# Optimization experiments

Hardware: AMD Instinct MI355X
Metric: run time of the kernel (lower is better)

## Reference

```python
import jax, jax.numpy as jnp
import numpy as np

N = 50000       # nodes
E = 500000      # edges (before self loops)
IN = 256        # in_dim
HID = 128       # hidden
HEADS = 2       # GATv2 heads (concat=False -> head mean)
G = 64          # num graphs in batch
SLOPE = 0.2     # leaky_relu negative slope (PyG default)


def setup_inputs() -> dict:
    key = jax.random.key(0)
    ks = jax.random.split(key, 30)
    w = lambda k, shape: jax.random.normal(k, shape, jnp.float32) * 0.05
    inp = {
        "x": jax.random.normal(ks[0], (N, IN), jnp.float32),
        "edge_index": jax.random.randint(ks[1], (2, E), 0, N, dtype=jnp.int64),
        "batch": jnp.sort(jax.random.randint(ks[2], (N,), 0, G, dtype=jnp.int64)),
        # encoder MLP
        "enc_w1": w(ks[3], (HID, IN)),  "enc_b1": w(ks[4], (HID,)),
        "enc_w2": w(ks[5], (HID, HID)), "enc_b2": w(ks[6], (HID,)),
        # GATv2 conv1: lin_l, lin_r -> heads*out; att [H, C]; final bias [C]
        "c1_wl": w(ks[7], (HEADS * HID, HID)),  "c1_bl": w(ks[8], (HEADS * HID,)),
        "c1_wr": w(ks[9], (HEADS * HID, HID)),  "c1_br": w(ks[10], (HEADS * HID,)),
        "c1_att": w(ks[11], (HEADS, HID)),       "c1_bias": w(ks[12], (HID,)),
        # GATv2 conv2
        "c2_wl": w(ks[13], (HEADS * HID, HID)), "c2_bl": w(ks[14], (HEADS * HID,)),
        "c2_wr": w(ks[15], (HEADS * HID, HID)), "c2_br": w(ks[16], (HEADS * HID,)),
        "c2_att": w(ks[17], (HEADS, HID)),       "c2_bias": w(ks[18], (HID,)),
        # attentional pooling gate MLP
        "gate_w1": w(ks[19], (HID, HID)), "gate_b1": w(ks[20], (HID,)),
        "gate_w2": w(ks[21], (1, HID)),   "gate_b2": w(ks[22], (1,)),
        # head MLP
        "head_w1": w(ks[23], (HID, HID)), "head_b1": w(ks[24], (HID,)),
        "head_w2": w(ks[25], (2, HID)),   "head_b2": w(ks[26], (2,)),
    }
    return inp


def _gatv2(x, src, dst, wl, bl, wr, br, att, bias):
    """PyG GATv2Conv, heads=HEADS, concat=False (mean over heads)."""
    n = x.shape[0]
    xl = (x @ wl.T + bl).reshape(n, HEADS, HID)   # source transform
    xr = (x @ wr.T + br).reshape(n, HEADS, HID)   # target transform
    s = jax.nn.leaky_relu(xl[src] + xr[dst], SLOPE)          # [E,H,C]
    e = jnp.einsum('ehc,hc->eh', s, att)                      # [E,H]
    m = jax.ops.segment_max(e, dst, num_segments=n)
    a = jnp.exp(e - m[dst])
    a = a / (jax.ops.segment_sum(a, dst, num_segments=n)[dst] + 1e-16)
    out = jax.ops.segment_sum(a[:, :, None] * xl[src], dst, num_segments=n)
    return out.mean(axis=1) + bias                            # [N,C]


def _forward(x, edge_index, batch,
             enc_w1, enc_b1, enc_w2, enc_b2,
             c1_wl, c1_bl, c1_wr, c1_br, c1_att, c1_bias,
             c2_wl, c2_bl, c2_wr, c2_br, c2_att, c2_bias,
             gate_w1, gate_b1, gate_w2, gate_b2,
             head_w1, head_b1, head_w2, head_b2):
    n = x.shape[0]
    # add self loops (PyG GATv2Conv default add_self_loops=True)
    loop = jnp.arange(n, dtype=edge_index.dtype)
    src = jnp.concatenate([edge_index[0], loop])
    dst = jnp.concatenate([edge_index[1], loop])

    h = jax.nn.relu(x @ enc_w1.T + enc_b1)
    h = jax.nn.relu(h @ enc_w2.T + enc_b2)
    h = jax.nn.relu(_gatv2(h, src, dst, c1_wl, c1_bl, c1_wr, c1_br, c1_att, c1_bias))
    h = jax.nn.relu(_gatv2(h, src, dst, c2_wl, c2_bl, c2_wr, c2_br, c2_att, c2_bias))

    # attentional aggregation: segment-softmax gate over graphs
    gate = (jax.nn.relu(h @ gate_w1.T + gate_b1) @ gate_w2.T + gate_b2)[:, 0]  # [N]
    gm = jax.ops.segment_max(gate, batch, num_segments=G)
    ga = jnp.exp(gate - gm[batch])
    ga = ga / (jax.ops.segment_sum(ga, batch, num_segments=G)[batch] + 1e-16)
    g = jax.ops.segment_sum(ga[:, None] * h, batch, num_segments=G)  # [G,HID]

    out = jax.nn.relu(g @ head_w1.T + head_b1) @ head_w2.T + head_b2  # [G,2]
    # F.normalize(dim=1), eps=1e-12
    norm = jnp.linalg.norm(out, axis=1, keepdims=True)
    return out / jnp.maximum(norm, 1e-12)


def reference(x, edge_index, batch,
              enc_w1, enc_b1, enc_w2, enc_b2,
              c1_wl, c1_bl, c1_wr, c1_br, c1_att, c1_bias,
              c2_wl, c2_bl, c2_wr, c2_br, c2_att, c2_bias,
              gate_w1, gate_b1, gate_w2, gate_b2,
              head_w1, head_b1, head_w2, head_b2):
    return _forward(x, edge_index, batch,
                    enc_w1, enc_b1, enc_w2, enc_b2,
                    c1_wl, c1_bl, c1_wr, c1_br, c1_att, c1_bias,
                    c2_wl, c2_bl, c2_wr, c2_br, c2_att, c2_bias,
                    gate_w1, gate_b1, gate_w2, gate_b2,
                    head_w1, head_b1, head_w2, head_b2)
```

## Files before the change

### kernel.cpp

```cpp
#include <hip/hip_runtime.h>
#include <math.h>

#define CH 128
#define F2 256
#define NG 64
#define PS 16

typedef __attribute__((ext_vector_type(8))) short short8;
typedef __attribute__((ext_vector_type(4))) float f32x4;

__device__ inline ushort f2bf_t(float x) { return (ushort)(__float_as_uint(x) >> 16); }
__device__ inline ushort f2bf_r(float x) {
  uint u = __float_as_uint(x);
  return (ushort)((u + 0x7fffu + ((u >> 16) & 1u)) >> 16);
}
__device__ inline float bf2f(ushort h) { return __uint_as_float(((uint)h) << 16); }

struct WSpec { const float* src; ushort* hi; ushort* lo; int n; };
struct WPack { WSpec w[7]; };
__global__ __launch_bounds__(256) void split_weights(WPack p) {
  const WSpec s = p.w[blockIdx.y];
  for (int i = blockIdx.x * 256 + threadIdx.x; i < s.n; i += gridDim.x * 256) {
    const float v = s.src[i];
    if (s.lo) {
      const ushort h = f2bf_t(v);
      s.hi[i] = h;
      s.lo[i] = f2bf_t(v - bf2f(h));
    } else {
      s.hi[i] = f2bf_r(v);
    }
  }
}

template<int NT, int ACT, int AF32, int GATE, int SPLIT, int WSPLIT>
__global__ __launch_bounds__(NT * 128) void gemm_full(
    const void* __restrict__ Av, const ushort* __restrict__ Whi,
    const ushort* __restrict__ Wlo, const float* __restrict__ bias,
    const float* __restrict__ bias2, ushort* __restrict__ Cb0,
    ushort* __restrict__ Cb1, const float* __restrict__ w2,
    const float* __restrict__ b2, float* __restrict__ gate, int M, int K) {
  constexpr int Nn = NT * 64;
  constexpr int NTH = NT * 128;
  constexpr int ACF = AF32 ? (1024 / NTH) : 1;
  constexpr int ACB = AF32 ? 1 : ((512 + NTH - 1) / NTH);
  extern __shared__ ushort smem[];
  ushort* Ab = smem;
  ushort* Wh = smem + 128 * 40;
  ushort* Wl = WSPLIT ? (Wh + Nn * 40) : Wh;
  const int tid = threadIdx.x;
  const int lane = tid & 63, wid = tid >> 6;
  const int wm = wid / NT, wn = wid % NT;
  const int bm = blockIdx.x * 128;
  const int fr = lane & 15, fg = lane >> 4;

  f32x4 acc[4][4];
#pragma unroll
  for (int i = 0; i < 4; ++i)
#pragma unroll
    for (int j = 0; j < 4; ++j) acc[i][j] = (f32x4)0.f;

  float4 avf[ACF];
  short8 avb[ACB];
  short8 wvh[2], wvl[2];
  auto load_tiles = [&](int k0) {
    if constexpr (AF32) {
#pragma unroll
      for (int i2 = 0; i2 < ACF; ++i2) {
        const int c = tid + NTH * i2;
        const int row = c >> 3, kq = (c & 7) * 4;
        const int gr = bm + row;
        avf[i2] = (gr < M) ? *(const float4*)((const float*)Av + (size_t)gr * K + k0 + kq)
                           : make_float4(0.f, 0.f, 0.f, 0.f);
      }
    } else {
#pragma unroll
      for (int i2 = 0; i2 < ACB; ++i2) {
        const int c = tid + NTH * i2;
        if (c < 512) {
          const int row = c >> 2, kq = (c & 3) * 8;
          const int gr = bm + row;
          avb[i2] = (gr < M) ? *(const short8*)((const ushort*)Av + (size_t)gr * K + k0 + kq)
                             : (short8)0;
        }
      }
    }
#pragma unroll
    for (int i2 = 0; i2 < 2; ++i2) {
      const int c = tid + NTH * i2;
      const int row = c >> 2, kq = (c & 3) * 8;
      wvh[i2] = *(const short8*)(Whi + (size_t)row * K + k0 + kq);
      if constexpr (WSPLIT)
        wvl[i2] = *(const short8*)(Wlo + (size_t)row * K + k0 + kq);
    }
  };

  load_tiles(0);
  for (int k0 = 0; k0 < K; k0 += 32) {
    __syncthreads();
    if constexpr (AF32) {
#pragma unroll
      for (int i2 = 0; i2 < ACF; ++i2) {
        const int c = tid + NTH * i2;
        const int row = c >> 3, kq = (c & 7) * 4;
        const float4 v = avf[i2];
        ushort4 h;
        h.x = f2bf_r(v.x); h.y = f2bf_r(v.y); h.z = f2bf_r(v.z); h.w = f2bf_r(v.w);
        *(ushort4*)&Ab[row * 40 + kq] = h;
      }
    } else {
#pragma unroll
      for (int i2 = 0; i2 < ACB; ++i2) {
        const int c = tid + NTH * i2;
        if (c < 512) {
          const int row = c >> 2, kq = (c & 3) * 8;
          *(short8*)&Ab[row * 40 + kq] = avb[i2];
        }
      }
    }
#pragma unroll
    for (int i2 = 0; i2 < 2; ++i2) {
      const int c = tid + NTH * i2;
      const int row = c >> 2, kq = (c & 3) * 8;
      *(short8*)&Wh[row * 40 + kq] = wvh[i2];
      if constexpr (WSPLIT) *(short8*)&Wl[row * 40 + kq] = wvl[i2];
    }
    __syncthreads();
    if (k0 + 32 < K) load_tiles(k0 + 32);
    short8 fa[4];
#pragma unroll
    for (int i = 0; i < 4; ++i)
      fa[i] = *(const short8*)&Ab[(wm * 64 + i * 16 + fr) * 40 + fg * 8];
#pragma unroll
    for (int j = 0; j < 4; ++j) {
      const int wbase = (wn * 64 + j * 16 + fr) * 40 + fg * 8;
      const short8 fwh = *(const short8*)&Wh[wbase];
#pragma unroll
      for (int i = 0; i < 4; ++i)
        acc[i][j] = __builtin_amdgcn_mfma_f32_16x16x32_bf16(fa[i], fwh, acc[i][j], 0, 0, 0);
      if constexpr (WSPLIT) {
        const short8 fwl = *(const short8*)&Wl[wbase];
#pragma unroll
        for (int i = 0; i < 4; ++i)
          acc[i][j] = __builtin_amdgcn_mfma_f32_16x16x32_bf16(fa[i], fwl, acc[i][j], 0, 0, 0);
      }
    }
  }
  if constexpr (GATE) {
    __shared__ float gpart[2][128];
    const float b2v = b2[0];
    float rsum[4][4];
#pragma unroll
    for (int i = 0; i < 4; ++i)
#pragma unroll
      for (int r = 0; r < 4; ++r) rsum[i][r] = 0.f;
#pragma unroll
    for (int j = 0; j < 4; ++j) {
      const int col = wn * 64 + j * 16 + fr;
      const float bv = bias[col], wv2 = w2[col];
#pragma unroll
      for (int i = 0; i < 4; ++i)
#pragma unroll
        for (int r = 0; r < 4; ++r) {
          const float v = fmaxf(acc[i][j][r] + bv, 0.f);
          rsum[i][r] += v * wv2;
        }
    }
#pragma unroll
    for (int i = 0; i < 4; ++i)
#pragma unroll
      for (int r = 0; r < 4; ++r) {
        float v = rsum[i][r];
        v += __shfl_xor(v, 1);
        v += __shfl_xor(v, 2);
        v += __shfl_xor(v, 4);
        v += __shfl_xor(v, 8);
        rsum[i][r] = v;
      }
    if (fr == 0) {
#pragma unroll
      for (int i = 0; i < 4; ++i)
#pragma unroll
        for (int r = 0; r < 4; ++r)
          gpart[wn][wm * 64 + i * 16 + fg * 4 + r] = rsum[i][r];
    }
    __syncthreads();
    if (tid < 128) {
      const int row = bm + tid;
      if (row < M) gate[row] = gpart[0][tid] + gpart[1][tid] + b2v;
    }
  } else {
#pragma unroll
    for (int j = 0; j < 4; ++j) {
      const int col = wn * 64 + j * 16 + fr;
      float bv;
      if constexpr (SPLIT) bv = (wn < NT / 2) ? bias[col] : bias2[col - Nn / 2];
      else                 bv = bias[col];
#pragma unroll
      for (int i = 0; i < 4; ++i)
#pragma unroll
        for (int r = 0; r < 4; ++r) {
          const int row = bm + wm * 64 + i * 16 + fg * 4 + r;
          if (row < M) {
            float v = acc[i][j][r] + bv;
            if (ACT) v = fmaxf(v, 0.f);
            const ushort o = f2bf_r(v);
            if constexpr (SPLIT) {
              if (wn < NT / 2) Cb0[(size_t)row * (Nn / 2) + col] = o;
              else             Cb1[(size_t)row * (Nn / 2) + col - Nn / 2] = o;
            } else {
              Cb0[(size_t)row * Nn + col] = o;
            }
          }
        }
    }
  }
}

__global__ void fill_zero_i32(int* __restrict__ p, int n) {
  int i = blockIdx.x * blockDim.x + threadIdx.x;
  if (i < n) p[i] = 0;
}
__global__ void edge_hist(const int* __restrict__ ei, int E, int Etot, int* __restrict__ counts) {
  int e = blockIdx.x * blockDim.x + threadIdx.x;
  if (e >= Etot) return;
  int d = (e < E) ? ei[E + e] : (e - E);
  atomicAdd(&counts[d], 1);
}
__global__ __launch_bounds__(1024) void hist_sums(const int* __restrict__ counts,
                                                  int* __restrict__ bsum, int n) {
  __shared__ int sm[1024];
  const int tid = threadIdx.x;
  const int idx = blockIdx.x * 1024 + tid;
  sm[tid] = (idx < n) ? counts[idx] : 0;
  __syncthreads();
  for (int off = 512; off; off >>= 1) {
    if (tid < off) sm[tid] += sm[tid + off];
    __syncthreads();
  }
  if (tid == 0) bsum[blockIdx.x] = sm[0];
}
__global__ void scan_bsums(const int* __restrict__ bsum, int* __restrict__ boff, int nb) {
  if (threadIdx.x == 0 && blockIdx.x == 0) {
    int run = 0;
    for (int i = 0; i < nb; ++i) { boff[i] = run; run += bsum[i]; }
  }
}
__global__ __launch_bounds__(1024) void scan_apply(const int* __restrict__ counts,
                                                   const int* __restrict__ boff,
                                                   int* __restrict__ indptr,
                                                   int* __restrict__ cur, int n) {
  __shared__ int sm[1024];
  const int tid = threadIdx.x;
  const int idx = blockIdx.x * 1024 + tid;
  const int v = (idx < n) ? counts[idx] : 0;
  sm[tid] = v;
  __syncthreads();
  for (int off = 1; off < 1024; off <<= 1) {
    const int t = (tid >= off) ? sm[tid - off] : 0;
    __syncthreads();
    sm[tid] += t;
    __syncthreads();
  }
  const int excl = boff[blockIdx.x] + sm[tid] - v;
  if (idx < n) {
    indptr[idx] = excl;
    cur[idx] = excl;
    if (idx == n - 1) indptr[n] = excl + v;
  }
}
__global__ void edge_scatter(const int* __restrict__ ei, int E, int Etot,
                             int* __restrict__ cur, int* __restrict__ csr_src) {
  int e = blockIdx.x * blockDim.x + threadIdx.x;
  if (e >= Etot) return;
  int s, d;
  if (e < E) { s = ei[e]; d = ei[E + e]; } else { s = e - E; d = s; }
  int p = atomicAdd(&cur[d], 1);
  csr_src[p] = s;
}

__global__ __launch_bounds__(256) void fused_conv(
    const int* __restrict__ indptr, const int* __restrict__ csr_src,
    const ushort* __restrict__ XLb, const ushort* __restrict__ XRb,
    const float* __restrict__ att, const float* __restrict__ bias,
    ushort* __restrict__ OUT, int N) {
  int node = (int)((blockIdx.x * (size_t)256 + threadIdx.x) >> 6);
  if (node >= N) return;
  const int lane = threadIdx.x & 63;
  const int f = lane * 4;
  const ushort4 xrb = *(const ushort4*)(XRb + (size_t)node * F2 + f);
  const float xr0 = bf2f(xrb.x), xr1 = bf2f(xrb.y), xr2 = bf2f(xrb.z), xr3 = bf2f(xrb.w);
  const float4 at = *(const float4*)(att + f);
  const int s = indptr[node], e = indptr[node + 1];
  float m = -3.4e38f, dsum = 0.f;
  float a0 = 0.f, a1 = 0.f, a2 = 0.f, a3 = 0.f;

  auto score = [&](float x0, float x1, float x2, float x3) -> float {
    float v0 = x0 + xr0; v0 = v0 > 0.f ? v0 : 0.2f * v0;
    float v1 = x1 + xr1; v1 = v1 > 0.f ? v1 : 0.2f * v1;
    float v2 = x2 + xr2; v2 = v2 > 0.f ? v2 : 0.2f * v2;
    float v3 = x3 + xr3; v3 = v3 > 0.f ? v3 : 0.2f * v3;
    return v0 * at.x + v1 * at.y + v2 * at.z + v3 * at.w;
  };
  auto update = [&](float p, float x0, float x1, float x2, float x3) {
    if (__all(p <= m)) {
      const float w = __expf(p - m);
      dsum += w;
      a0 += w * x0; a1 += w * x1; a2 += w * x2; a3 += w * x3;
    } else {
      const float mn = fmaxf(m, p);
      const float sc = __expf(m - mn);
      const float w  = __expf(p - mn);
      dsum = dsum * sc + w;
      a0 = a0 * sc + w * x0; a1 = a1 * sc + w * x1;
      a2 = a2 * sc + w * x2; a3 = a3 * sc + w * x3;
      m = mn;
    }
  };

  int k = s;
  for (; k + 4 <= e; k += 4) {
    const int sn0 = csr_src[k + 0];
    const int sn1 = csr_src[k + 1];
    const int sn2 = csr_src[k + 2];
    const int sn3 = csr_src[k + 3];
    const ushort4 b0 = *(const ushort4*)(XLb + (size_t)sn0 * F2 + f);
    const ushort4 b1 = *(const ushort4*)(XLb + (size_t)sn1 * F2 + f);
    const ushort4 b2 = *(const ushort4*)(XLb + (size_t)sn2 * F2 + f);
    const ushort4 b3 = *(const ushort4*)(XLb + (size_t)sn3 * F2 + f);
    const float x00 = bf2f(b0.x), x01 = bf2f(b0.y), x02 = bf2f(b0.z), x03 = bf2f(b0.w);
    const float x10 = bf2f(b1.x), x11 = bf2f(b1.y), x12 = bf2f(b1.z), x13 = bf2f(b1.w);
    const float x20 = bf2f(b2.x), x21 = bf2f(b2.y), x22 = bf2f(b2.z), x23 = bf2f(b2.w);
    const float x30 = bf2f(b3.x), x31 = bf2f(b3.y), x32 = bf2f(b3.z), x33 = bf2f(b3.w);
    float p0 = score(x00, x01, x02, x03);
    float p1 = score(x10, x11, x12, x13);
    float p2 = score(x20, x21, x22, x23);
    float p3 = score(x30, x31, x32, x33);
#pragma unroll
    for (int d2 = 1; d2 <= 16; d2 <<= 1) {
      p0 += __shfl_xor(p0, d2);
      p1 += __shfl_xor(p1, d2);
      p2 += __shfl_xor(p2, d2);
      p3 += __shfl_xor(p3, d2);
    }
    update(p0, x00, x01, x02, x03);
    update(p1, x10, x11, x12, x13);
    update(p2, x20, x21, x22, x23);
    update(p3, x30, x31, x32, x33);
  }
  for (; k < e; ++k) {
    const int sn = csr_src[k];
    const ushort4 xb = *(const ushort4*)(XLb + (size_t)sn * F2 + f);
    const float x0 = bf2f(xb.x), x1 = bf2f(xb.y), x2 = bf2f(xb.z), x3 = bf2f(xb.w);
    float p = score(x0, x1, x2, x3);
#pragma unroll
    for (int d2 = 1; d2 <= 16; d2 <<= 1) p += __shfl_xor(p, d2);
    update(p, x0, x1, x2, x3);
  }

  const float inv = 1.f / (dsum + 1e-16f);
  a0 *= inv; a1 *= inv; a2 *= inv; a3 *= inv;
  float o0 = 0.5f * (a0 + __shfl_xor(a0, 32));
  float o1 = 0.5f * (a1 + __shfl_xor(a1, 32));
  float o2 = 0.5f * (a2 + __shfl_xor(a2, 32));
  float o3 = 0.5f * (a3 + __shfl_xor(a3, 32));
  if (lane < 32) {
    ushort4 r;
    r.x = f2bf_r(fmaxf(o0 + bias[f + 0], 0.f));
    r.y = f2bf_r(fmaxf(o1 + bias[f + 1], 0.f));
    r.z = f2bf_r(fmaxf(o2 + bias[f + 2], 0.f));
    r.w = f2bf_r(fmaxf(o3 + bias[f + 3], 0.f));
    *(ushort4*)(OUT + (size_t)node * CH + f) = r;
  }
}

__global__ __launch_bounds__(256) void pool_stats(
    const float* __restrict__ gate, const int* __restrict__ batch,
    float* __restrict__ pm, float* __restrict__ pd, int N) {
  const int g = blockIdx.x, tid = threadIdx.x;
  int lo = 0, hi = N;
  while (lo < hi) { int mid = (lo + hi) >> 1; if (batch[mid] < g) lo = mid + 1; else hi = mid; }
  const int s = lo;
  lo = 0; hi = N;
  while (lo < hi) { int mid = (lo + hi) >> 1; if (batch[mid] < g + 1) lo = mid + 1; else hi = mid; }
  const int e = lo;
  __shared__ float red[256];
  float m = -3.4e38f;
  for (int n = s + tid; n < e; n += 256) m = fmaxf(m, gate[n]);
  red[tid] = m; __syncthreads();
  for (int off = 128; off; off >>= 1) {
    if (tid < off) red[tid] = fmaxf(red[tid], red[tid + off]);
    __syncthreads();
  }
  m = red[0]; __syncthreads();
  float d = 0.f;
  for (int n = s + tid; n < e; n += 256) d += expf(gate[n] - m);
  red[tid] = d; __syncthreads();
  for (int off = 128; off; off >>= 1) {
    if (tid < off) red[tid] += red[tid + off];
    __syncthreads();
  }
  if (tid == 0) { pm[g] = m; pd[g] = red[0]; }
}

__global__ __launch_bounds__(128) void pool_partial(
    const float* __restrict__ gate, const int* __restrict__ batch,
    const float* __restrict__ pm, const float* __restrict__ pd,
    const ushort* __restrict__ H, float* __restrict__ PART, int N) {
  const int g = blockIdx.x / PS, j = blockIdx.x % PS;
  const int tid = threadIdx.x;
  int lo = 0, hi = N;
  while (lo < hi) { int mid = (lo + hi) >> 1; if (batch[mid] < g) lo = mid + 1; else hi = mid; }
  const int s = lo;
  lo = 0; hi = N;
  while (lo < hi) { int mid = (lo + hi) >> 1; if (batch[mid] < g + 1) lo = mid + 1; else hi = mid; }
  const int e = lo;
  const int len = e - s;
  const int per = (len + PS - 1) / PS;
  const int ns = s + j * per;
  const int ne = min(ns + per, e);
  const float m = pm[g];
  const float inv = 1.f / (pd[g] + 1e-16f);
  float acc = 0.f;
  for (int n = ns; n < ne; ++n) {
    const float w = expf(gate[n] - m);
    acc += w * bf2f(H[(size_t)n * CH + tid]);
  }
  PART[(size_t)blockIdx.x * CH + tid] = acc * inv;
}
__global__ __launch_bounds__(128) void pool_reduce(
    const float* __restrict__ PART, float* __restrict__ Gout) {
  const int g = blockIdx.x, tid = threadIdx.x;
  float acc = 0.f;
#pragma unroll
  for (int j = 0; j < PS; ++j) acc += PART[(size_t)(g * PS + j) * CH + tid];
  Gout[(size_t)g * CH + tid] = acc;
}

__global__ __launch_bounds__(128) void head_kernel(
    const float* __restrict__ Gin, const float* __restrict__ w1, const float* __restrict__ b1,
    const float* __restrict__ w2, const float* __restrict__ b2, float* __restrict__ out) {
  const int g = blockIdx.x, tid = threadIdx.x;
  __shared__ float gs[128], ts[128], o[2];
  gs[tid] = Gin[(size_t)g * CH + tid];
  __syncthreads();
  float a = b1[tid];
  for (int k = 0; k < CH; ++k) a += w1[tid * CH + k] * gs[k];
  ts[tid] = fmaxf(a, 0.f);
  __syncthreads();
  if (tid < 2) {
    float v = b2[tid];
    for (int d2 = 0; d2 < CH; ++d2) v += w2[tid * CH + d2] * ts[d2];
    o[tid] = v;
  }
  __syncthreads();
  if (tid == 0) {
    float nrm = sqrtf(o[0] * o[0] + o[1] * o[1]);
    nrm = fmaxf(nrm, 1e-12f);
    out[g * 2 + 0] = o[0] / nrm;
    out[g * 2 + 1] = o[1] / nrm;
  }
}

extern "C" void kernel_launch(void* const* d_in, const int* in_sizes, int n_in,
                              void* d_out, int out_size, void* d_ws, size_t ws_size,
                              hipStream_t stream) {
  const float* x       = (const float*)d_in[0];
  const int*   ei      = (const int*)d_in[1];
  const int*   batch   = (const int*)d_in[2];
  const float* enc_w1  = (const float*)d_in[3];
  const float* enc_b1  = (const float*)d_in[4];
  const float* enc_w2  = (const float*)d_in[5];
  const float* enc_b2  = (const float*)d_in[6];
  const float* c1_wl   = (const float*)d_in[7];
  const float* c1_bl   = (const float*)d_in[8];
  const float* c1_wr   = (const float*)d_in[9];
  const float* c1_br   = (const float*)d_in[10];
  const float* c1_att  = (const float*)d_in[11];
  const float* c1_bias = (const float*)d_in[12];
  const float* c2_wl   = (const float*)d_in[13];
  const float* c2_bl   = (const float*)d_in[14];
  const float* c2_wr   = (const float*)d_in[15];
  const float* c2_br   = (const float*)d_in[16];
  const float* c2_att  = (const float*)d_in[17];
  const float* c2_bias = (const float*)d_in[18];
  const float* gate_w1 = (const float*)d_in[19];
  const float* gate_b1 = (const float*)d_in[20];
  const float* gate_w2 = (const float*)d_in[21];
  const float* gate_b2 = (const float*)d_in[22];
  const float* head_w1 = (const float*)d_in[23];
  const float* head_b1 = (const float*)d_in[24];
  const float* head_w2 = (const float*)d_in[25];
  const float* head_b2 = (const float*)d_in[26];

  const int N    = in_sizes[2];
  const int E    = in_sizes[1] / 2;
  const int INF_ = in_sizes[0] / N;
  const int Etot = E + N;
  const int NBLK = (N + 1023) / 1024;

  char* wp = (char*)d_ws;
  auto alloc = [&](size_t bytes) -> void* {
    void* p = (void*)wp;
    wp += (bytes + 255) & ~(size_t)255;
    return p;
  };
  ushort* XLb    = (ushort*)alloc((size_t)N * F2 * 2);
  ushort* XRb    = (ushort*)alloc((size_t)N * F2 * 2);
  ushort* Ha     = (ushort*)alloc((size_t)N * CH * 2);
  ushort* Hb     = (ushort*)alloc((size_t)N * CH * 2);
  ushort* Hc     = (ushort*)alloc((size_t)N * CH * 2);
  int*    counts = (int*)alloc((size_t)N * 4);
  int*    indptr = (int*)alloc((size_t)(N + 1) * 4);
  int*    cur    = (int*)alloc((size_t)N * 4);
  int*    csr_src= (int*)alloc((size_t)Etot * 4);
  int*    bsum   = (int*)alloc((size_t)NBLK * 4);
  int*    boff   = (int*)alloc((size_t)NBLK * 4);
  float*  gateb  = (float*)alloc((size_t)N * 4);
  float*  GS     = (float*)alloc((size_t)NG * CH * 4);
  float*  pm     = (float*)alloc((size_t)NG * 4);
  float*  pd     = (float*)alloc((size_t)NG * 4);
  float*  PART   = (float*)alloc((size_t)NG * PS * CH * 4);
  ushort* We1h = (ushort*)alloc((size_t)CH * INF_ * 2);
  ushort* We1l = (ushort*)alloc((size_t)CH * INF_ * 2);
  ushort* We2h = (ushort*)alloc((size_t)CH * CH * 2);
  ushort* We2l = (ushort*)alloc((size_t)CH * CH * 2);
  ushort* Wc1  = (ushort*)alloc((size_t)2 * F2 * CH * 2);
  ushort* Wc2  = (ushort*)alloc((size_t)2 * F2 * CH * 2);
  ushort* Wgh  = (ushort*)alloc((size_t)CH * CH * 2);
  ushort* Wgl  = (ushort*)alloc((size_t)CH * CH * 2);

  const dim3 blk(256);
  const int gM = (N + 127) / 128;
  const int nw = F2 * CH;

  WPack wpk;
  wpk.w[0] = { enc_w1,  We1h,       We1l,    CH * INF_ };
  wpk.w[1] = { enc_w2,  We2h,       We2l,    CH * CH };
  wpk.w[2] = { c1_wl,   Wc1,        nullptr, nw };
  wpk.w[3] = { c1_wr,   Wc1 + nw,   nullptr, nw };
  wpk.w[4] = { c2_wl,   Wc2,        nullptr, nw };
  wpk.w[5] = { c2_wr,   Wc2 + nw,   nullptr, nw };
  wpk.w[6] = { gate_w1, Wgh,        Wgl,     CH * CH };
  split_weights<<<dim3(128, 7), blk, 0, stream>>>(wpk);

  const int LDS2 = (128 * 40 + 2 * 128 * 40) * 2;
  const int LDS8 = (128 * 40 + 512 * 40) * 2;

  fill_zero_i32<<<(N + 255) / 256, blk, 0, stream>>>(counts, N);
  edge_hist<<<(Etot + 255) / 256, blk, 0, stream>>>(ei, E, Etot, counts);
  hist_sums<<<NBLK, 1024, 0, stream>>>(counts, bsum, N);
  scan_bsums<<<1, 64, 0, stream>>>(bsum, boff, NBLK);
  scan_apply<<<NBLK, 1024, 0, stream>>>(counts, boff, indptr, cur, N);
  edge_scatter<<<(Etot + 255) / 256, blk, 0, stream>>>(ei, E, Etot, cur, csr_src);

  gemm_full<2,1,1,0,0,1><<<gM, 256, LDS2, stream>>>(
      x, We1h, We1l, enc_b1, nullptr, Ha, nullptr, nullptr, nullptr, nullptr, N, INF_);
  gemm_full<2,1,0,0,0,1><<<gM, 256, LDS2, stream>>>(
      Ha, We2h, We2l, enc_b2, nullptr, Hb, nullptr, nullptr, nullptr, nullptr, N, CH);

  gemm_full<8,0,0,0,1,0><<<gM, 1024, LDS8, stream>>>(
      Hb, Wc1, nullptr, c1_bl, c1_br, XLb, XRb, nullptr, nullptr, nullptr, N, CH);
  fused_conv<<<(N + 3) / 4, blk, 0, stream>>>(indptr, csr_src, XLb, XRb, c1_att, c1_bias, Hc, N);

  gemm_full<8,0,0,0,1,0><<<gM, 1024, LDS8, stream>>>(
      Hc, Wc2, nullptr, c2_bl, c2_br, XLb, XRb, nullptr, nullptr, nullptr, N, CH);
  fused_conv<<<(N + 3) / 4, blk, 0, stream>>>(indptr, csr_src, XLb, XRb, c2_att, c2_bias, Hb, N);

  gemm_full<2,1,0,1,0,1><<<gM, 256, LDS2, stream>>>(
      Hb, Wgh, Wgl, gate_b1, nullptr, nullptr, nullptr, gate_w2, gate_b2, gateb, N, CH);

  pool_stats<<<NG, blk, 0, stream>>>(gateb, batch, pm, pd, N);
  pool_partial<<<NG * PS, 128, 0, stream>>>(gateb, batch, pm, pd, Hb, PART, N);
  pool_reduce<<<NG, 128, 0, stream>>>(PART, GS);

  head_kernel<<<NG, 128, 0, stream>>>(GS, head_w1, head_b1, head_w2, head_b2, (float*)d_out);
}
```

Baseline: 489.0 us.

## Retile GEMMs for more waves, fuse pooling stats and reduce into neighbors

The 128-wide GEMMs now run 8 waves per block, each holding a 32x64 sub-tile instead of 4 waves holding 64x64. The conv projection GEMM uses 64-row tiles with 1024 threads so the grid has twice as many blocks. Pooling statistics are recomputed inside each partial block, and the partial-sum reduction moves into the head kernel, removing two launches. Leaky-relu becomes a fmax form. The cost is redundant max/sum work across the 16 partial blocks per graph and more weight reloads per block.

```diff
diff --git a/kernel.cpp b/kernel.cpp
--- a/kernel.cpp
+++ b/kernel.cpp
@@ -32,65 +32,51 @@
   }
 }
 
-template<int NT, int ACT, int AF32, int GATE, int SPLIT, int WSPLIT>
-__global__ __launch_bounds__(NT * 128) void gemm_full(
+template<int ACT, int AF32, int GATE>
+__global__ __launch_bounds__(512) void gemm128(
     const void* __restrict__ Av, const ushort* __restrict__ Whi,
     const ushort* __restrict__ Wlo, const float* __restrict__ bias,
-    const float* __restrict__ bias2, ushort* __restrict__ Cb0,
-    ushort* __restrict__ Cb1, const float* __restrict__ w2,
+    ushort* __restrict__ Cb, const float* __restrict__ w2,
     const float* __restrict__ b2, float* __restrict__ gate, int M, int K) {
-  constexpr int Nn = NT * 64;
-  constexpr int NTH = NT * 128;
-  constexpr int ACF = AF32 ? (1024 / NTH) : 1;
-  constexpr int ACB = AF32 ? 1 : ((512 + NTH - 1) / NTH);
   extern __shared__ ushort smem[];
   ushort* Ab = smem;
   ushort* Wh = smem + 128 * 40;
-  ushort* Wl = WSPLIT ? (Wh + Nn * 40) : Wh;
+  ushort* Wl = Wh + 128 * 40;
   const int tid = threadIdx.x;
   const int lane = tid & 63, wid = tid >> 6;
-  const int wm = wid / NT, wn = wid % NT;
+  const int wm = wid >> 1, wn = wid & 1;
   const int bm = blockIdx.x * 128;
   const int fr = lane & 15, fg = lane >> 4;
 
-  f32x4 acc[4][4];
-#pragma unroll
-  for (int i = 0; i < 4; ++i)
+  f32x4 acc[2][4];
+#pragma unroll
+  for (int i = 0; i < 2; ++i)
 #pragma unroll
     for (int j = 0; j < 4; ++j) acc[i][j] = (f32x4)0.f;
 
-  float4 avf[ACF];
-  short8 avb[ACB];
-  short8 wvh[2], wvl[2];
+  float4 avf[2];
+  short8 avb;
+  short8 wvh, wvl;
   auto load_tiles = [&](int k0) {
     if constexpr (AF32) {
 #pragma unroll
-      for (int i2 = 0; i2 < ACF; ++i2) {
-        const int c = tid + NTH * i2;
+      for (int i2 = 0; i2 < 2; ++i2) {
+        const int c = tid + 512 * i2;
         const int row = c >> 3, kq = (c & 7) * 4;
         const int gr = bm + row;
         avf[i2] = (gr < M) ? *(const float4*)((const float*)Av + (size_t)gr * K + k0 + kq)
                            : make_float4(0.f, 0.f, 0.f, 0.f);
       }
     } else {
-#pragma unroll
-      for (int i2 = 0; i2 < ACB; ++i2) {
-        const int c = tid + NTH * i2;
-        if (c < 512) {
-          const int row = c >> 2, kq = (c & 3) * 8;
-          const int gr = bm + row;
-          avb[i2] = (gr < M) ? *(const short8*)((const ushort*)Av + (size_t)gr * K + k0 + kq)
-                             : (short8)0;
-        }
-      }
-    }
-#pragma unroll
-    for (int i2 = 0; i2 < 2; ++i2) {
-      const int c = tid + NTH * i2;
-      const int row = c >> 2, kq = (c & 3) * 8;
-      wvh[i2] = *(const short8*)(Whi + (size_t)row * K + k0 + kq);
-      if constexpr (WSPLIT)
-        wvl[i2] = *(const short8*)(Wlo + (size_t)row * K + k0 + kq);
+      const int row = tid >> 2, kq = (tid & 3) * 8;
+      const int gr = bm + row;
+      avb = (gr < M) ? *(const short8*)((const ushort*)Av + (size_t)gr * K + k0 + kq)
+                     : (short8)0;
+    }
+    {
+      const int row = tid >> 2, kq = (tid & 3) * 8;
+      wvh = *(const short8*)(Whi + (size_t)row * K + k0 + kq);
+      wvl = *(const short8*)(Wlo + (size_t)row * K + k0 + kq);
     }
   };
 
@@ -99,8 +85,8 @@
     __syncthreads();
     if constexpr (AF32) {
 #pragma unroll
-      for (int i2 = 0; i2 < ACF; ++i2) {
-        const int c = tid + NTH * i2;
+      for (int i2 = 0; i2 < 2; ++i2) {
+        const int c = tid + 512 * i2;
         const int row = c >> 3, kq = (c & 7) * 4;
         const float4 v = avf[i2];
         ushort4 h;
@@ -108,49 +94,38 @@
         *(ushort4*)&Ab[row * 40 + kq] = h;
       }
     } else {
-#pragma unroll
-      for (int i2 = 0; i2 < ACB; ++i2) {
-        const int c = tid + NTH * i2;
-        if (c < 512) {
-          const int row = c >> 2, kq = (c & 3) * 8;
-          *(short8*)&Ab[row * 40 + kq] = avb[i2];
-        }
-      }
-    }
-#pragma unroll
-    for (int i2 = 0; i2 < 2; ++i2) {
-      const int c = tid + NTH * i2;
-      const int row = c >> 2, kq = (c & 3) * 8;
-      *(short8*)&Wh[row * 40 + kq] = wvh[i2];
-      if constexpr (WSPLIT) *(short8*)&Wl[row * 40 + kq] = wvl[i2];
+      const int row = tid >> 2, kq = (tid & 3) * 8;
+      *(short8*)&Ab[row * 40 + kq] = avb;
+    }
+    {
+      const int row = tid >> 2, kq = (tid & 3) * 8;
+      *(short8*)&Wh[row * 40 + kq] = wvh;
+      *(short8*)&Wl[row * 40 + kq] = wvl;
     }
     __syncthreads();
     if (k0 + 32 < K) load_tiles(k0 + 32);
-    short8 fa[4];
-#pragma unroll
-    for (int i = 0; i < 4; ++i)
-      fa[i] = *(const short8*)&Ab[(wm * 64 + i * 16 + fr) * 40 + fg * 8];
+    short8 fa[2];
+#pragma unroll
+    for (int i = 0; i < 2; ++i)
+      fa[i] = *(const short8*)&Ab[(wm * 32 + i * 16 + fr) * 40 + fg * 8];
 #pragma unroll
     for (int j = 0; j < 4; ++j) {
       const int wbase = (wn * 64 + j * 16 + fr) * 40 + fg * 8;
       const short8 fwh = *(const short8*)&Wh[wbase];
-#pragma unroll
-      for (int i = 0; i < 4; ++i)
+      const short8 fwl = *(const short8*)&Wl[wbase];
+#pragma unroll
+      for (int i = 0; i < 2; ++i) {
         acc[i][j] = __builtin_amdgcn_mfma_f32_16x16x32_bf16(fa[i], fwh, acc[i][j], 0, 0, 0);
-      if constexpr (WSPLIT) {
-        const short8 fwl = *(const short8*)&Wl[wbase];
-#pragma unroll
-        for (int i = 0; i < 4; ++i)
-          acc[i][j] = __builtin_amdgcn_mfma_f32_16x16x32_bf16(fa[i], fwl, acc[i][j], 0, 0, 0);
+        acc[i][j] = __builtin_amdgcn_mfma_f32_16x16x32_bf16(fa[i], fwl, acc[i][j], 0, 0, 0);
       }
     }
   }
   if constexpr (GATE) {
     __shared__ float gpart[2][128];
     const float b2v = b2[0];
-    float rsum[4][4];
-#pragma unroll
-    for (int i = 0; i < 4; ++i)
+    float rsum[2][4];
+#pragma unroll
+    for (int i = 0; i < 2; ++i)
 #pragma unroll
       for (int r = 0; r < 4; ++r) rsum[i][r] = 0.f;
 #pragma unroll
@@ -158,7 +133,7 @@
       const int col = wn * 64 + j * 16 + fr;
       const float bv = bias[col], wv2 = w2[col];
 #pragma unroll
-      for (int i = 0; i < 4; ++i)
+      for (int i = 0; i < 2; ++i)
 #pragma unroll
         for (int r = 0; r < 4; ++r) {
           const float v = fmaxf(acc[i][j][r] + bv, 0.f);
@@ -166,7 +141,7 @@
         }
     }
 #pragma unroll
-    for (int i = 0; i < 4; ++i)
+    for (int i = 0; i < 2; ++i)
 #pragma unroll
       for (int r = 0; r < 4; ++r) {
         float v = rsum[i][r];
@@ -178,10 +153,10 @@
       }
     if (fr == 0) {
 #pragma unroll
-      for (int i = 0; i < 4; ++i)
+      for (int i = 0; i < 2; ++i)
 #pragma unroll
         for (int r = 0; r < 4; ++r)
-          gpart[wn][wm * 64 + i * 16 + fg * 4 + r] = rsum[i][r];
+          gpart[wn][wm * 32 + i * 16 + fg * 4 + r] = rsum[i][r];
     }
     __syncthreads();
     if (tid < 128) {
@@ -192,27 +167,98 @@
 #pragma unroll
     for (int j = 0; j < 4; ++j) {
       const int col = wn * 64 + j * 16 + fr;
-      float bv;
-      if constexpr (SPLIT) bv = (wn < NT / 2) ? bias[col] : bias2[col - Nn / 2];
-      else                 bv = bias[col];
-#pragma unroll
-      for (int i = 0; i < 4; ++i)
+      const float bv = bias[col];
+#pragma unroll
+      for (int i = 0; i < 2; ++i)
 #pragma unroll
         for (int r = 0; r < 4; ++r) {
-          const int row = bm + wm * 64 + i * 16 + fg * 4 + r;
+          const int row = bm + wm * 32 + i * 16 + fg * 4 + r;
           if (row < M) {
             float v = acc[i][j][r] + bv;
             if (ACT) v = fmaxf(v, 0.f);
-            const ushort o = f2bf_r(v);
-            if constexpr (SPLIT) {
-              if (wn < NT / 2) Cb0[(size_t)row * (Nn / 2) + col] = o;
-              else             Cb1[(size_t)row * (Nn / 2) + col - Nn / 2] = o;
-            } else {
-              Cb0[(size_t)row * Nn + col] = o;
-            }
+            Cb[(size_t)row * 128 + col] = f2bf_r(v);
           }
         }
     }
+  }
+}
+
+__global__ __launch_bounds__(1024) void gemm_conv(
+    const ushort* __restrict__ A, const ushort* __restrict__ W,
+    const float* __restrict__ bl, const float* __restrict__ br,
+    ushort* __restrict__ XLb, ushort* __restrict__ XRb, int M, int K) {
+  extern __shared__ ushort smem[];
+  ushort* Ab = smem;
+  ushort* Wh = smem + 64 * 40;
+  const int tid = threadIdx.x;
+  const int lane = tid & 63, wid = tid >> 6;
+  const int bm = blockIdx.x * 64;
+  const int fr = lane & 15, fg = lane >> 4;
+
+  f32x4 acc[4][2];
+#pragma unroll
+  for (int i = 0; i < 4; ++i)
+#pragma unroll
+    for (int j = 0; j < 2; ++j) acc[i][j] = (f32x4)0.f;
+
+  short8 avb;
+  short8 wv[2];
+  auto load_tiles = [&](int k0) {
+    if (tid < 256) {
+      const int row = tid >> 2, kq = (tid & 3) * 8;
+      const int gr = bm + row;
+      avb = (gr < M) ? *(const short8*)(A + (size_t)gr * K + k0 + kq) : (short8)0;
+    }
+#pragma unroll
+    for (int i2 = 0; i2 < 2; ++i2) {
+      const int c = tid + 1024 * i2;
+      const int row = c >> 2, kq = (c & 3) * 8;
+      wv[i2] = *(const short8*)(W + (size_t)row * K + k0 + kq);
+    }
+  };
+
+  load_tiles(0);
+  for (int k0 = 0; k0 < K; k0 += 32) {
+    __syncthreads();
+    if (tid < 256) {
+      const int row = tid >> 2, kq = (tid & 3) * 8;
+      *(short8*)&Ab[row * 40 + kq] = avb;
+    }
+#pragma unroll
+    for (int i2 = 0; i2 < 2; ++i2) {
+      const int c = tid + 1024 * i2;
+      const int row = c >> 2, kq = (c & 3) * 8;
+      *(short8*)&Wh[row * 40 + kq] = wv[i2];
+    }
+    __syncthreads();
+    if (k0 + 32 < K) load_tiles(k0 + 32);
+    short8 fa[4];
+#pragma unroll
+    for (int i = 0; i < 4; ++i)
+      fa[i] = *(const short8*)&Ab[(i * 16 + fr) * 40 + fg * 8];
+#pragma unroll
+    for (int j = 0; j < 2; ++j) {
+      const short8 fw = *(const short8*)&Wh[(wid * 32 + j * 16 + fr) * 40 + fg * 8];
+#pragma unroll
+      for (int i = 0; i < 4; ++i)
+        acc[i][j] = __builtin_amdgcn_mfma_f32_16x16x32_bf16(fa[i], fw, acc[i][j], 0, 0, 0);
+    }
+  }
+#pragma unroll
+  for (int j = 0; j < 2; ++j) {
+    const int col = wid * 32 + j * 16 + fr;
+    const float bv = (col < 256) ? bl[col] : br[col - 256];
+#pragma unroll
+    for (int i = 0; i < 4; ++i)
+#pragma unroll
+      for (int r = 0; r < 4; ++r) {
+        const int row = bm + i * 16 + fg * 4 + r;
+        if (row < M) {
+          const ushort o = f2bf_r(acc[i][j][r] + bv);
+          if (col < 256) XLb[(size_t)row * 256 + col] = o;
+          else           XRb[(size_t)row * 256 + col - 256] = o;
+        }
+      }
   }
 }
 
@@ -295,10 +341,10 @@
   float a0 = 0.f, a1 = 0.f, a2 = 0.f, a3 = 0.f;
 
   auto score = [&](float x0, float x1, float x2, float x3) -> float {
-    float v0 = x0 + xr0; v0 = v0 > 0.f ? v0 : 0.2f * v0;
-    float v1 = x1 + xr1; v1 = v1 > 0.f ? v1 : 0.2f * v1;
-    float v2 = x2 + xr2; v2 = v2 > 0.f ? v2 : 0.2f * v2;
-    float v3 = x3 + xr3; v3 = v3 > 0.f ? v3 : 0.2f * v3;
+    const float v0 = fmaxf(x0 + xr0, 0.2f * (x0 + xr0));
+    const float v1 = fmaxf(x1 + xr1, 0.2f * (x1 + xr1));
+    const float v2 = fmaxf(x2 + xr2, 0.2f * (x2 + xr2));
+    const float v3 = fmaxf(x3 + xr3, 0.2f * (x3 + xr3));
     return v0 * at.x + v1 * at.y + v2 * at.z + v3 * at.w;
   };
   auto update = [&](float p, float x0, float x1, float x2, float x3) {
@@ -373,38 +419,8 @@
   }
 }
 
-__global__ __launch_bounds__(256) void pool_stats(
-    const float* __restrict__ gate, const int* __restrict__ batch,
-    float* __restrict__ pm, float* __restrict__ pd, int N) {
-  const int g = blockIdx.x, tid = threadIdx.x;
-  int lo = 0, hi = N;
-  while (lo < hi) { int mid = (lo + hi) >> 1; if (batch[mid] < g) lo = mid + 1; else hi = mid; }
-  const int s = lo;
-  lo = 0; hi = N;
-  while (lo < hi) { int mid = (lo + hi) >> 1; if (batch[mid] < g + 1) lo = mid + 1; else hi = mid; }
-  const int e = lo;
-  __shared__ float red[256];
-  float m = -3.4e38f;
-  for (int n = s + tid; n < e; n += 256) m = fmaxf(m, gate[n]);
-  red[tid] = m; __syncthreads();
-  for (int off = 128; off; off >>= 1) {
-    if (tid < off) red[tid] = fmaxf(red[tid], red[tid + off]);
-    __syncthreads();
-  }
-  m = red[0]; __syncthreads();
-  float d = 0.f;
-  for (int n = s + tid; n < e; n += 256) d += expf(gate[n] - m);
-  red[tid] = d; __syncthreads();
-  for (int off = 128; off; off >>= 1) {
-    if (tid < off) red[tid] += red[tid + off];
-    __syncthreads();
-  }
-  if (tid == 0) { pm[g] = m; pd[g] = red[0]; }
-}
-
 __global__ __launch_bounds__(128) void pool_partial(
     const float* __restrict__ gate, const int* __restrict__ batch,
-    const float* __restrict__ pm, const float* __restrict__ pd,
     const ushort* __restrict__ H, float* __restrict__ PART, int N) {
   const int g = blockIdx.x / PS, j = blockIdx.x % PS;
   const int tid = threadIdx.x;
@@ -414,12 +430,27 @@
   lo = 0; hi = N;
   while (lo < hi) { int mid = (lo + hi) >> 1; if (batch[mid] < g + 1) lo = mid + 1; else hi = mid; }
   const int e = lo;
+  __shared__ float red[128];
+  float m = -3.4e38f;
+  for (int n = s + tid; n < e; n += 128) m = fmaxf(m, gate[n]);
+  red[tid] = m; __syncthreads();
+  for (int off = 64; off; off >>= 1) {
+    if (tid < off) red[tid] = fmaxf(red[tid], red[tid + off]);
+    __syncthreads();
+  }
+  m = red[0]; __syncthreads();
+  float d = 0.f;
+  for (int n = s + tid; n < e; n += 128) d += expf(gate[n] - m);
+  red[tid] = d; __syncthreads();
+  for (int off = 64; off; off >>= 1) {
+    if (tid < off) red[tid] += red[tid + off];
+    __syncthreads();
+  }
+  const float inv = 1.f / (red[0] + 1e-16f);
   const int len = e - s;
   const int per = (len + PS - 1) / PS;
   const int ns = s + j * per;
   const int ne = min(ns + per, e);
-  const float m = pm[g];
-  const float inv = 1.f / (pd[g] + 1e-16f);
   float acc = 0.f;
   for (int n = ns; n < ne; ++n) {
     const float w = expf(gate[n] - m);
@@ -427,21 +458,16 @@
   }
   PART[(size_t)blockIdx.x * CH + tid] = acc * inv;
 }
-__global__ __launch_bounds__(128) void pool_reduce(
-    const float* __restrict__ PART, float* __restrict__ Gout) {
-  const int g = blockIdx.x, tid = threadIdx.x;
-  float acc = 0.f;
-#pragma unroll
-  for (int j = 0; j < PS; ++j) acc += PART[(size_t)(g * PS + j) * CH + tid];
-  Gout[(size_t)g * CH + tid] = acc;
-}
 
 __global__ __launch_bounds__(128) void head_kernel(
-    const float* __restrict__ Gin, const float* __restrict__ w1, const float* __restrict__ b1,
+    const float* __restrict__ PART, const float* __restrict__ w1, const float* __restrict__ b1,
     const float* __restrict__ w2, const float* __restrict__ b2, float* __restrict__ out) {
   const int g = blockIdx.x, tid = threadIdx.x;
   __shared__ float gs[128], ts[128], o[2];
-  gs[tid] = Gin[(size_t)g * CH + tid];
+  float gsum = 0.f;
+#pragma unroll
+  for (int j = 0; j < PS; ++j) gsum += PART[(size_t)(g * PS + j) * CH + tid];
+  gs[tid] = gsum;
   __syncthreads();
   float a = b1[tid];
   for (int k = 0; k < CH; ++k) a += w1[tid * CH + k] * gs[k];
@@ -516,9 +542,6 @@
   int*    bsum   = (int*)alloc((size_t)NBLK * 4);
   int*    boff   = (int*)alloc((size_t)NBLK * 4);
   float*  gateb  = (float*)alloc((size_t)N * 4);
-  float*  GS     = (float*)alloc((size_t)NG * CH * 4);
-  float*  pm     = (float*)alloc((size_t)NG * 4);
-  float*  pd     = (float*)alloc((size_t)NG * 4);
   float*  PART   = (float*)alloc((size_t)NG * PS * CH * 4);
   ushort* We1h = (ushort*)alloc((size_t)CH * INF_ * 2);
   ushort* We1l = (ushort*)alloc((size_t)CH * INF_ * 2);
@@ -530,7 +553,8 @@
   ushort* Wgl  = (ushort*)alloc((size_t)CH * CH * 2);
 
   const dim3 blk(256);
-  const int gM = (N + 127) / 128;
+  const int gM128 = (N + 127) / 128;
+  const int gM64  = (N + 63) / 64;
   const int nw = F2 * CH;
 
   WPack wpk;
@@ -543,8 +567,8 @@
   wpk.w[6] = { gate_w1, Wgh,        Wgl,     CH * CH };
   split_weights<<<dim3(128, 7), blk, 0, stream>>>(wpk);
 
-  const int LDS2 = (128 * 40 + 2 * 128 * 40) * 2;
-  const int LDS8 = (128 * 40 + 512 * 40) * 2;
+  const int LDS128  = (128 * 40 * 3) * 2;
+  const int LDSCONV = (64 * 40 + 512 * 40) * 2;
 
   fill_zero_i32<<<(N + 255) / 256, blk, 0, stream>>>(counts, N);
   edge_hist<<<(Etot + 255) / 256, blk, 0, stream>>>(ei, E, Etot, counts);
@@ -553,25 +577,21 @@
   scan_apply<<<NBLK, 1024, 0, stream>>>(counts, boff, indptr, cur, N);
   edge_scatter<<<(Etot + 255) / 256, blk, 0, stream>>>(ei, E, Etot, cur, csr_src);
 
-  gemm_full<2,1,1,0,0,1><<<gM, 256, LDS2, stream>>>(
-      x, We1h, We1l, enc_b1, nullptr, Ha, nullptr, nullptr, nullptr, nullptr, N, INF_);
-  gemm_full<2,1,0,0,0,1><<<gM, 256, LDS2, stream>>>(
-      Ha, We2h, We2l, enc_b2, nullptr, Hb, nullptr, nullptr, nullptr, nullptr, N, CH);
-
-  gemm_full<8,0,0,0,1,0><<<gM, 1024, LDS8, stream>>>(
-      Hb, Wc1, nullptr, c1_bl, c1_br, XLb, XRb, nullptr, nullptr, nullptr, N, CH);
+  gemm128<1,1,0><<<gM128, 512, LDS128, stream>>>(
+      x, We1h, We1l, enc_b1, Ha, nullptr, nullptr, nullptr, N, INF_);
+  gemm128<1,0,0><<<gM128, 512, LDS128, stream>>>(
+      Ha, We2h, We2l, enc_b2, Hb, nullptr, nullptr, nullptr, N, CH);
+
+  gemm_conv<<<gM64, 1024, LDSCONV, stream>>>(Hb, Wc1, c1_bl, c1_br, XLb, XRb, N, CH);
   fused_conv<<<(N + 3) / 4, blk, 0, stream>>>(indptr, csr_src, XLb, XRb, c1_att, c1_bias, Hc, N);
 
-  gemm_full<8,0,0,0,1,0><<<gM, 1024, LDS8, stream>>>(
-      Hc, Wc2, nullptr, c2_bl, c2_br, XLb, XRb, nullptr, nullptr, nullptr, N, CH);
+  gemm_conv<<<gM64, 1024, LDSCONV, stream>>>(Hc, Wc2, c2_bl, c2_br, XLb, XRb, N, CH);
   fused_conv<<<(N + 3) / 4, blk, 0, stream>>>(indptr, csr_src, XLb, XRb, c2_att, c2_bias, Hb, N);
 
-  gemm_full<2,1,0,1,0,1><<<gM, 256, LDS2, stream>>>(
-      Hb, Wgh, Wgl, gate_b1, nullptr, nullptr, nullptr, gate_w2, gate_b2, gateb, N, CH);
-
-  pool_stats<<<NG, blk, 0, stream>>>(gateb, batch, pm, pd, N);
-  pool_partial<<<NG * PS, 128, 0, stream>>>(gateb, batch, pm, pd, Hb, PART, N);
-  pool_reduce<<<NG, 128, 0, stream>>>(PART, GS);
-
-  head_kernel<<<NG, 128, 0, stream>>>(GS, head_w1, head_b1, head_w2, head_b2, (float*)d_out);
-}
+  gemm128<1,0,1><<<gM128, 512, LDS128, stream>>>(
+      Hb, Wgh, Wgl, gate_b1, nullptr, gate_w2, gate_b2, gateb, N, CH);
+
+  pool_partial<<<NG * PS, 128, 0, stream>>>(gateb, batch, Hb, PART, N);
+
+  head_kernel<<<NG, 128, 0, stream>>>(PART, head_w1, head_b1, head_w2, head_b2, (float*)d_out);
+}
```

After: 472.9 us. 1.03x faster.
